# Kernel optimization log

Hardware: AMD Instinct MI355X
Metric: run time of the kernel (lower is better)

Reference implementation:

```python
import jax, jax.numpy as jnp
import numpy as np

B, S, H, D = 4, 2048, 16, 64
DM = H * D  # model dim 1024


def _rope_sincos(seq_len, d2):
    # sin/cos tables for the rotated sub-dimension d2 (= head_dim // 2)
    inv_freq = 1.0 / (10000.0 ** (jnp.arange(0, d2, 2, dtype=jnp.float32) / d2))
    ang = jnp.arange(seq_len, dtype=jnp.float32)[:, None] * inv_freq[None, :]  # (S, d2/2)
    emb = jnp.concatenate([ang, ang], axis=-1)  # (S, d2)
    return jnp.sin(emb), jnp.cos(emb)


def _apply_rope(x, sin, cos):
    # x: (B, S, H, D). Only the first half of head_dim is rotated (faithful to
    # apply_rotary_pos_emb: split -> rotate x1 -> concat with untouched x2).
    x1, x2 = jnp.split(x, 2, axis=-1)  # each (B, S, H, D//2)
    a, b = jnp.split(x1, 2, axis=-1)
    rot = jnp.concatenate([-b, a], axis=-1)  # rotate_half(x1)
    sin = sin[None, :, None, :]
    cos = cos[None, :, None, :]
    return jnp.concatenate([x1 * cos + rot * sin, x2], axis=-1)


def setup_inputs() -> dict:
    key = jax.random.key(0)
    k1, k2 = jax.random.split(key)
    x = jax.random.normal(k1, (B, S, DM), dtype=jnp.float32)
    w_qkv = jax.random.normal(k2, (DM, 3 * H * D), dtype=jnp.float32) / np.sqrt(DM).astype(np.float32)
    mask = jnp.tril(jnp.ones((1, 1, S, S), dtype=bool))  # causal
    return {"x": x, "w_qkv": w_qkv, "mask": mask}


def reference(x, w_qkv, mask):
    b, s, _ = x.shape
    qkv = x @ w_qkv  # (B, S, 3*H*D) fused QKV projection (no bias)
    q, k, v = jnp.split(qkv, 3, axis=-1)
    q = q.reshape(b, s, H, D)
    k = k.reshape(b, s, H, D)
    v = v.reshape(b, s, H, D)
    sin, cos = _rope_sincos(s, D // 2)
    q = _apply_rope(q, sin, cos)
    k = _apply_rope(k, sin, cos)
    # full (B, H, S, S) score matrix, scaled by sqrt(head_dim)
    attn = jnp.einsum('bqhd,bkhd->bhqk', q, k) / jnp.sqrt(jnp.float32(D))
    attn = jnp.where(mask, attn, -jnp.inf)
    attn = jax.nn.softmax(attn, axis=-1)
    out = jnp.einsum('bhqk,bkhd->bqhd', attn, v)
    return out.reshape(b, s, H * D)
```

## Files before the change

### kernel.cpp

```cpp
#include <hip/hip_runtime.h>
#include <hip/hip_bf16.h>

#define SEQ 2048
#define DM 1024
#define NOUT 3072

typedef __attribute__((ext_vector_type(8))) short bf16x8;
typedef __attribute__((ext_vector_type(4))) float f32x4;
typedef __attribute__((ext_vector_type(16))) float f32x16;
typedef __attribute__((ext_vector_type(4))) unsigned int u32x4;

__device__ inline unsigned short bfb(float f) {
    __hip_bfloat16 h = __float2bfloat16(f);
    return __builtin_bit_cast(unsigned short, h);
}

__device__ inline unsigned pk2(float lo, float hi) {
    return (unsigned)bfb(lo) | ((unsigned)bfb(hi) << 16);
}

__device__ inline void gload_lds16(const void* g, void* l) {
    __builtin_amdgcn_global_load_lds(
        (const __attribute__((address_space(1))) unsigned int*)g,
        (__attribute__((address_space(3))) unsigned int*)l, 16, 0, 0);
}

#define M3(a, b, c) fmaxf(fmaxf((a), (b)), (c))

__global__ __launch_bounds__(256) void prep_kernel(
    const float* __restrict__ x, __hip_bfloat16* __restrict__ xb,
    const float* __restrict__ w, __hip_bfloat16* __restrict__ wT,
    float* __restrict__ sintab, float* __restrict__ costab) {
    __shared__ float t[64][65];
    const int b = blockIdx.x, tid = threadIdx.x;
    if (b < 8192) {
        int i = b * 256 + tid;
        float4 v = ((const float4*)x)[i];
        ushort4 o;
        o.x = bfb(v.x); o.y = bfb(v.y); o.z = bfb(v.z); o.w = bfb(v.w);
        ((ushort4*)xb)[i] = o;
    } else if (b < 8960) {
        const int idx = b - 8192;
        const int k0 = (idx & 15) * 64;
        const int n0 = (idx >> 4) * 64;
        for (int i = tid; i < 4096; i += 256) {
            int r = i >> 6, c = i & 63;
            t[r][c] = w[(size_t)(k0 + r) * NOUT + n0 + c];
        }
        __syncthreads();
        for (int i = tid; i < 4096; i += 256) {
            int nl = i >> 6, kl = i & 63;
            wT[(size_t)(n0 + nl) * DM + k0 + kl] = __float2bfloat16(t[kl][nl]);
        }
    } else {
        int i = (b - 8960) * 256 + tid;
        int f = i & 15, s = i >> 4;
        float inv = powf(10000.0f, -(float)f * (1.0f / 16.0f));
        float ang = (float)s * inv;
        sintab[i] = sinf(ang);
        costab[i] = cosf(ang);
    }
}

#define BM 128
#define BN 128
#define BK 32

__global__ __launch_bounds__(256) void qkv_gemm_kernel(
    const __hip_bfloat16* __restrict__ xb, const __hip_bfloat16* __restrict__ wT,
    const float* __restrict__ costab, const float* __restrict__ sintab,
    __hip_bfloat16* __restrict__ Qg, __hip_bfloat16* __restrict__ Kg,
    __hip_bfloat16* __restrict__ Vt) {
    __shared__ __hip_bfloat16 As[BM * BK];
    __shared__ __hip_bfloat16 Bs[BN * BK];
    const int tid = threadIdx.x, lane = tid & 63, wid = tid >> 6;
    const int wm = wid >> 1, wn = wid & 1;
    const int m0 = blockIdx.x * BM, n0 = blockIdx.y * BN;
    const int g = lane >> 4;

    f32x4 acc[4][4] = {};

    for (int k0 = 0; k0 < DM; k0 += BK) {
        __syncthreads();
#pragma unroll
        for (int c2 = 0; c2 < 2; ++c2) {
            const int chunk = wid * 2 + c2;
            gload_lds16(xb + (size_t)(m0 + chunk * 16 + (lane >> 2)) * DM + k0 + (lane & 3) * 8,
                        &As[chunk * 512]);
            gload_lds16(wT + (size_t)(n0 + chunk * 16 + (lane >> 2)) * DM + k0 + (lane & 3) * 8,
                        &Bs[chunk * 512]);
        }
        __syncthreads();
        bf16x8 a[4], b[4];
#pragma unroll
        for (int mf = 0; mf < 4; ++mf)
            a[mf] = *(const bf16x8*)&As[(wm * 64 + mf * 16 + (lane & 15)) * BK + (g << 3)];
#pragma unroll
        for (int nf = 0; nf < 4; ++nf)
            b[nf] = *(const bf16x8*)&Bs[(wn * 64 + nf * 16 + (lane & 15)) * BK + (g << 3)];
#pragma unroll
        for (int mf = 0; mf < 4; ++mf)
#pragma unroll
            for (int nf = 0; nf < 4; ++nf)
                acc[mf][nf] = __builtin_amdgcn_mfma_f32_16x16x32_bf16(a[mf], b[nf], acc[mf][nf], 0, 0, 0);
    }

    const int colbase = n0 + wn * 64;
    const int part = colbase >> 10;
    const int h = (colbase & 1023) >> 6;
    const int d0 = lane & 15;
    const int rowg0 = m0 + wm * 64 + (g << 2);

    if (part == 2) {
#pragma unroll
        for (int mf = 0; mf < 4; ++mf) {
            const int rbase = rowg0 + mf * 16;
            const int b = rbase >> 11, s = rbase & 2047;
            const size_t vb = (size_t)(b * 16 + h) * 64 * SEQ;
#pragma unroll
            for (int nf = 0; nf < 4; ++nf) {
                const int d = nf * 16 + d0;
                ushort4 pk;
                pk.x = bfb(acc[mf][nf][0]);
                pk.y = bfb(acc[mf][nf][1]);
                pk.z = bfb(acc[mf][nf][2]);
                pk.w = bfb(acc[mf][nf][3]);
                *(ushort4*)((unsigned short*)Vt + vb + (size_t)d * SEQ + s) = pk;
            }
        }
    } else {
        __hip_bfloat16* __restrict__ dstT = part ? Kg : Qg;
        const float sc = part ? 1.0f : 0.125f * 1.44269504088896340736f;
#pragma unroll
        for (int mf = 0; mf < 4; ++mf) {
#pragma unroll
            for (int j = 0; j < 4; ++j) {
                const int mg = rowg0 + mf * 16 + j;
                const int b = mg >> 11, s = mg & 2047;
                const float cv = costab[s * 16 + d0];
                const float sv = sintab[s * 16 + d0];
                const float v0 = acc[mf][0][j], v1 = acc[mf][1][j];
                __hip_bfloat16* dst = dstT + ((size_t)(b * 16 + h) * SEQ + s) * 64;
                dst[d0]      = __float2bfloat16((v0 * cv - v1 * sv) * sc);
                dst[16 + d0] = __float2bfloat16((v1 * cv + v0 * sv) * sc);
                dst[32 + d0] = __float2bfloat16(acc[mf][2][j] * sc);
                dst[48 + d0] = __float2bfloat16(acc[mf][3][j] * sc);
            }
        }
    }
}

__global__ __launch_bounds__(512) void attn_fwd_kernel(
    const __hip_bfloat16* __restrict__ Qg, const __hip_bfloat16* __restrict__ Kg,
    const __hip_bfloat16* __restrict__ Vt, float* __restrict__ out) {
    __shared__ __align__(16) char smem[2][16384];
    const int tid = threadIdx.x, lane = tid & 63, wid = tid >> 6;
    const int qt = 7 - (blockIdx.x >> 6);
    const int bh = blockIdx.x & 63;
    const size_t base = (size_t)bh << 17;
    const int ql = lane & 31, hi = lane >> 5;
    const int qb = (qt << 8) + (wid << 5);
    const int qrow = qb + ql;
    const int nkt = 4 * qt + 4;
    const unsigned short* Kgu = (const unsigned short*)Kg + base;
    const unsigned short* Vtu = (const unsigned short*)Vt + base;
    const int b = bh >> 4, h = bh & 15;
    const int lo16 = lane << 4;

    bf16x8 qfrag[4];
    {
        const unsigned short* qp = (const unsigned short*)Qg + base + (size_t)qrow * 64 + hi * 8;
#pragma unroll
        for (int c = 0; c < 4; ++c) qfrag[c] = *(const bf16x8*)(qp + c * 16);
    }

    f32x16 accO[2] = {};
    float m = -INFINITY, l = 0.0f;

    const int ci0 = (wid & 3) * 2;
    const unsigned short* stsrc;
    int stdst;
    if (wid < 4) {
        stsrc = Kgu + (size_t)((ci0 >> 2) * 32 + ql) * 64 + (ci0 & 3) * 16 + hi * 8;
        stdst = ci0 * 1024;
    } else {
        stsrc = Vtu + (size_t)((ci0 >> 2) * 32 + ql) * SEQ + (ci0 & 3) * 16 + hi * 8;
        stdst = 8192 + ci0 * 1024;
    }

    {
#pragma unroll
        for (int c = 0; c < 2; ++c)
            gload_lds16(stsrc + c * 16, &smem[0][stdst + c * 1024]);
    }

    int cur = 0;
#pragma unroll 1
    for (int kt = 0; kt < nkt; ++kt) {
        const int k0 = kt << 6;
        if (kt + 1 < nkt) {
            const int kn = (kt + 1) << 6;
            const unsigned short* sn = (wid < 4) ? stsrc + (size_t)kn * 64 : stsrc + kn;
            char* nb = &smem[cur ^ 1][stdst];
#pragma unroll
            for (int c = 0; c < 2; ++c)
                gload_lds16(sn + c * 16, nb + c * 1024);
            asm volatile("s_waitcnt vmcnt(2)" ::: "memory");
        } else {
            asm volatile("s_waitcnt vmcnt(0)" ::: "memory");
        }
        __builtin_amdgcn_s_barrier();
        __builtin_amdgcn_sched_barrier(0);

        if (k0 <= qb + 31) {
            const char* Ks = smem[cur];
            const char* Vs = smem[cur] + 8192;

            f32x16 st[2] = {};
            __builtin_amdgcn_s_setprio(1);
#pragma unroll
            for (int c = 0; c < 4; ++c) {
                bf16x8 kf0 = *(const bf16x8*)(Ks + c * 1024 + lo16);
                bf16x8 kf1 = *(const bf16x8*)(Ks + 4096 + c * 1024 + lo16);
                st[0] = __builtin_amdgcn_mfma_f32_32x32x16_bf16(kf0, qfrag[c], st[0], 0, 0, 0);
                st[1] = __builtin_amdgcn_mfma_f32_32x32x16_bf16(kf1, qfrag[c], st[1], 0, 0, 0);
            }
            __builtin_amdgcn_s_setprio(0);

            if (k0 + 63 > qb) {
#pragma unroll
                for (int t = 0; t < 2; ++t)
#pragma unroll
                    for (int r = 0; r < 16; ++r) {
                        const int kg = k0 + 32 * t + (r & 3) + 8 * (r >> 2) + 4 * hi;
                        if (kg > qrow) st[t][r] = -INFINITY;
                    }
            }

            float x0 = M3(st[0][0], st[0][1], st[0][2]);
            float x1 = M3(st[0][3], st[0][4], st[0][5]);
            float x2 = M3(st[0][6], st[0][7], st[0][8]);
            float x3 = M3(st[0][9], st[0][10], st[0][11]);
            float x4 = M3(st[0][12], st[0][13], st[0][14]);
            float x5 = M3(st[0][15], st[1][0], st[1][1]);
            float x6 = M3(st[1][2], st[1][3], st[1][4]);
            float x7 = M3(st[1][5], st[1][6], st[1][7]);
            float x8 = M3(st[1][8], st[1][9], st[1][10]);
            float x9 = M3(st[1][11], st[1][12], st[1][13]);
            float xa = fmaxf(st[1][14], st[1][15]);
            float y0 = M3(x0, x1, x2), y1 = M3(x3, x4, x5);
            float y2 = M3(x6, x7, x8), y3 = M3(x9, xa, y0);
            float tm = M3(y1, y2, y3);
            tm = fmaxf(tm, __shfl_xor(tm, 32, 64));

            if (__any(tm > m + 8.0f)) {
                const float mn = fmaxf(m, tm);
                const float scl = __builtin_amdgcn_exp2f(m - mn);
                m = mn;
                l *= scl;
#pragma unroll
                for (int db = 0; db < 2; ++db)
#pragma unroll
                    for (int r = 0; r < 16; ++r) accO[db][r] *= scl;
            }

            float s0 = 0.0f, s1 = 0.0f, s2 = 0.0f, s3 = 0.0f;
#pragma unroll
            for (int r = 0; r < 16; r += 4) {
                float p00 = __builtin_amdgcn_exp2f(st[0][r + 0] - m);
                float p01 = __builtin_amdgcn_exp2f(st[0][r + 1] - m);
                float p02 = __builtin_amdgcn_exp2f(st[0][r + 2] - m);
                float p03 = __builtin_amdgcn_exp2f(st[0][r + 3] - m);
                float p10 = __builtin_amdgcn_exp2f(st[1][r + 0] - m);
                float p11 = __builtin_amdgcn_exp2f(st[1][r + 1] - m);
                float p12 = __builtin_amdgcn_exp2f(st[1][r + 2] - m);
                float p13 = __builtin_amdgcn_exp2f(st[1][r + 3] - m);
                st[0][r + 0] = p00; st[0][r + 1] = p01; st[0][r + 2] = p02; st[0][r + 3] = p03;
                st[1][r + 0] = p10; st[1][r + 1] = p11; st[1][r + 2] = p12; st[1][r + 3] = p13;
                s0 += p00 + p01; s1 += p02 + p03;
                s2 += p10 + p11; s3 += p12 + p13;
            }
            float ls = (s0 + s1) + (s2 + s3);
            ls += __shfl_xor(ls, 32, 64);
            l += ls;

            bf16x8 pfrag[4];
#pragma unroll
            for (int ks = 0; ks < 4; ++ks) {
                const int t = ks >> 1, rb = (ks & 1) * 8;
                unsigned a0 = pk2(st[t][rb + 0], st[t][rb + 1]);
                unsigned a1 = pk2(st[t][rb + 2], st[t][rb + 3]);
                unsigned b0 = pk2(st[t][rb + 4], st[t][rb + 5]);
                unsigned b1 = pk2(st[t][rb + 6], st[t][rb + 7]);
                asm("v_permlane32_swap_b32 %0, %1" : "+v"(a0), "+v"(b0));
                asm("v_permlane32_swap_b32 %0, %1" : "+v"(a1), "+v"(b1));
                u32x4 w;
                w[0] = a0;
                w[1] = a1;
                w[2] = b0;
                w[3] = b1;
                pfrag[ks] = __builtin_bit_cast(bf16x8, w);
            }

            __builtin_amdgcn_s_setprio(1);
#pragma unroll
            for (int ks = 0; ks < 4; ++ks) {
#pragma unroll
                for (int db = 0; db < 2; ++db) {
                    bf16x8 vf = *(const bf16x8*)(Vs + (db * 4 + ks) * 1024 + lo16);
                    accO[db] = __builtin_amdgcn_mfma_f32_32x32x16_bf16(vf, pfrag[ks], accO[db], 0, 0, 0);
                }
            }
            __builtin_amdgcn_s_setprio(0);
        }

        __builtin_amdgcn_sched_barrier(0);
        __builtin_amdgcn_s_barrier();
        cur ^= 1;
    }

    const float invl = 1.0f / l;
    float* orow = out + (size_t)(b * SEQ + qrow) * DM + h * 64;
#pragma unroll
    for (int db = 0; db < 2; ++db)
#pragma unroll
        for (int rg = 0; rg < 4; ++rg) {
            float4 v;
            v.x = accO[db][rg * 4 + 0] * invl;
            v.y = accO[db][rg * 4 + 1] * invl;
            v.z = accO[db][rg * 4 + 2] * invl;
            v.w = accO[db][rg * 4 + 3] * invl;
            *(float4*)(orow + db * 32 + rg * 8 + hi * 4) = v;
        }
}

extern "C" void kernel_launch(void* const* d_in, const int* in_sizes, int n_in,
                              void* d_out, int out_size, void* d_ws, size_t ws_size,
                              hipStream_t stream) {
    const float* x = (const float*)d_in[0];
    const float* w = (const float*)d_in[1];
    float* out = (float*)d_out;
    char* ws = (char*)d_ws;

    __hip_bfloat16* xb  = (__hip_bfloat16*)(ws + 0);
    __hip_bfloat16* wT  = (__hip_bfloat16*)(ws + 16777216);
    __hip_bfloat16* Qg  = (__hip_bfloat16*)(ws + 23068672);
    __hip_bfloat16* Kg  = (__hip_bfloat16*)(ws + 39845888);
    __hip_bfloat16* Vt  = (__hip_bfloat16*)(ws + 56623104);
    float* costab       = (float*)(ws + 73400320);
    float* sintab       = (float*)(ws + 73531392);

    prep_kernel<<<dim3(9088), dim3(256), 0, stream>>>(x, xb, w, wT, sintab, costab);
    qkv_gemm_kernel<<<dim3(64, 24), dim3(256), 0, stream>>>(xb, wT, costab, sintab, Qg, Kg, Vt);
    attn_fwd_kernel<<<dim3(512), dim3(512), 0, stream>>>(Qg, Kg, Vt, out);
}
```

Before: 141.6 us.

## Rewrite QKV GEMM as 256x256 double-buffered, swizzled, 8-wave pipelined kernel

Replaces the 128x128x32 single-buffered QKV projection GEMM with 256x256 tiles, BK=64, 8 waves and 128KB of dynamic LDS split into two buffers. Global-to-LDS loads for the next K step are issued in quarters between MFMA phases, with explicit vmcnt waits, barriers and raised priority around the MFMA blocks. An XOR swizzle is added to cut LDS bank conflicts. The aim is to hide load latency and increase data reuse per tile, at the cost of only 384 blocks (one per CU), which may leave CUs underused.

```diff
diff --git a/kernel.cpp b/kernel.cpp
--- a/kernel.cpp
+++ b/kernel.cpp
@@ -62,58 +62,151 @@
     }
 }
 
-#define BM 128
-#define BN 128
-#define BK 32
-
-__global__ __launch_bounds__(256) void qkv_gemm_kernel(
+#define QPERBUF 65536
+
+__global__ __launch_bounds__(512, 1) void qkv_gemm_kernel(
     const __hip_bfloat16* __restrict__ xb, const __hip_bfloat16* __restrict__ wT,
     const float* __restrict__ costab, const float* __restrict__ sintab,
     __hip_bfloat16* __restrict__ Qg, __hip_bfloat16* __restrict__ Kg,
     __hip_bfloat16* __restrict__ Vt) {
-    __shared__ __hip_bfloat16 As[BM * BK];
-    __shared__ __hip_bfloat16 Bs[BN * BK];
+    extern __shared__ __align__(16) char smc[];
     const int tid = threadIdx.x, lane = tid & 63, wid = tid >> 6;
-    const int wm = wid >> 1, wn = wid & 1;
-    const int m0 = blockIdx.x * BM, n0 = blockIdx.y * BN;
-    const int g = lane >> 4;
-
-    f32x4 acc[4][4] = {};
-
-    for (int k0 = 0; k0 < DM; k0 += BK) {
-        __syncthreads();
-#pragma unroll
-        for (int c2 = 0; c2 < 2; ++c2) {
-            const int chunk = wid * 2 + c2;
-            gload_lds16(xb + (size_t)(m0 + chunk * 16 + (lane >> 2)) * DM + k0 + (lane & 3) * 8,
-                        &As[chunk * 512]);
-            gload_lds16(wT + (size_t)(n0 + chunk * 16 + (lane >> 2)) * DM + k0 + (lane & 3) * 8,
-                        &Bs[chunk * 512]);
-        }
-        __syncthreads();
-        bf16x8 a[4], b[4];
-#pragma unroll
-        for (int mf = 0; mf < 4; ++mf)
-            a[mf] = *(const bf16x8*)&As[(wm * 64 + mf * 16 + (lane & 15)) * BK + (g << 3)];
-#pragma unroll
-        for (int nf = 0; nf < 4; ++nf)
-            b[nf] = *(const bf16x8*)&Bs[(wn * 64 + nf * 16 + (lane & 15)) * BK + (g << 3)];
-#pragma unroll
-        for (int mf = 0; mf < 4; ++mf)
-#pragma unroll
-            for (int nf = 0; nf < 4; ++nf)
-                acc[mf][nf] = __builtin_amdgcn_mfma_f32_16x16x32_bf16(a[mf], b[nf], acc[mf][nf], 0, 0, 0);
+    const int wm = wid >> 2, wn = wid & 3;
+    const int m0 = blockIdx.x * 256, n0 = blockIdx.y * 256;
+    const int l15 = lane & 15;
+
+    const int ak0 = (((lane >> 4) ^ (lane & 7)) << 4);
+    const int ak1 = (((4 + (lane >> 4)) ^ (lane & 7)) << 4);
+    const int Aoff = wm * 16384 + l15 * 128;
+    const int Boff = 32768 + (wn >> 1) * 16384 + (wn & 1) * 8192 + l15 * 128;
+
+    const int srow = lane >> 3;
+    const int skel = ((lane & 7) ^ srow) * 8;
+    const __hip_bfloat16* gA = xb + (size_t)(m0 + srow) * DM + skel;
+    const __hip_bfloat16* gB = wT + (size_t)(n0 + srow) * DM + skel;
+
+#define STAGE_A(h, l, kk, nb)                                                   \
+    gload_lds16(gA + (size_t)((h) * 128 + (l) * 64 + wid * 8) * DM + (kk),      \
+                smc + (nb) + (h) * 16384 + (l) * 8192 + wid * 1024)
+#define STAGE_B(h, l, kk, nb)                                                   \
+    gload_lds16(gB + (size_t)((h) * 128 + (l) * 64 + wid * 8) * DM + (kk),      \
+                smc + (nb) + 32768 + (h) * 16384 + (l) * 8192 + wid * 1024)
+
+    f32x4 acc[8][4] = {};
+    bf16x8 aR[4][2], bA[2][2], bB[2][2];
+
+    STAGE_A(0, 0, 0, 0); STAGE_A(0, 1, 0, 0);
+    STAGE_A(1, 0, 0, 0); STAGE_A(1, 1, 0, 0);
+    STAGE_B(0, 0, 0, 0); STAGE_B(0, 1, 0, 0);
+    STAGE_B(1, 0, 0, 0); STAGE_B(1, 1, 0, 0);
+
+#pragma unroll 1
+    for (int t = 0; t < 16; ++t) {
+        const int cb = (t & 1) * QPERBUF;
+        const int nb = cb ^ QPERBUF;
+        const int kk = (t + 1) * 64;
+        const char* Ab = smc + cb + Aoff;
+        const char* Bb = smc + cb + Boff;
+
+        if (t < 15) {
+            STAGE_A(0, 0, kk, nb); STAGE_A(0, 1, kk, nb);
+            asm volatile("s_waitcnt vmcnt(2)" ::: "memory");
+        } else {
+            asm volatile("s_waitcnt vmcnt(0)" ::: "memory");
+        }
+        __builtin_amdgcn_s_barrier();
+        __builtin_amdgcn_sched_barrier(0);
+#pragma unroll
+        for (int i = 0; i < 4; ++i) {
+            aR[i][0] = *(const bf16x8*)(Ab + i * 2048 + ak0);
+            aR[i][1] = *(const bf16x8*)(Ab + i * 2048 + ak1);
+        }
+#pragma unroll
+        for (int j = 0; j < 2; ++j) {
+            bA[j][0] = *(const bf16x8*)(Bb + j * 2048 + ak0);
+            bA[j][1] = *(const bf16x8*)(Bb + j * 2048 + ak1);
+        }
+        __builtin_amdgcn_s_setprio(1);
+#pragma unroll
+        for (int s = 0; s < 2; ++s)
+#pragma unroll
+            for (int i = 0; i < 4; ++i)
+#pragma unroll
+                for (int j = 0; j < 2; ++j)
+                    acc[i][j] = __builtin_amdgcn_mfma_f32_16x16x32_bf16(aR[i][s], bA[j][s], acc[i][j], 0, 0, 0);
+        __builtin_amdgcn_s_setprio(0);
+        __builtin_amdgcn_sched_barrier(0);
+        __builtin_amdgcn_s_barrier();
+        __builtin_amdgcn_sched_barrier(0);
+
+        if (t < 15) { STAGE_A(1, 0, kk, nb); STAGE_A(1, 1, kk, nb); }
+#pragma unroll
+        for (int j = 0; j < 2; ++j) {
+            bB[j][0] = *(const bf16x8*)(Bb + (2 + j) * 2048 + ak0);
+            bB[j][1] = *(const bf16x8*)(Bb + (2 + j) * 2048 + ak1);
+        }
+        __builtin_amdgcn_s_setprio(1);
+#pragma unroll
+        for (int s = 0; s < 2; ++s)
+#pragma unroll
+            for (int i = 0; i < 4; ++i)
+#pragma unroll
+                for (int j = 0; j < 2; ++j)
+                    acc[i][2 + j] = __builtin_amdgcn_mfma_f32_16x16x32_bf16(aR[i][s], bB[j][s], acc[i][2 + j], 0, 0, 0);
+        __builtin_amdgcn_s_setprio(0);
+        __builtin_amdgcn_sched_barrier(0);
+        __builtin_amdgcn_s_barrier();
+        __builtin_amdgcn_sched_barrier(0);
+
+        if (t < 15) { STAGE_B(0, 0, kk, nb); STAGE_B(0, 1, kk, nb); }
+#pragma unroll
+        for (int i = 0; i < 4; ++i) {
+            aR[i][0] = *(const bf16x8*)(Ab + (4 + i) * 2048 + ak0);
+            aR[i][1] = *(const bf16x8*)(Ab + (4 + i) * 2048 + ak1);
+        }
+#pragma unroll
+        for (int j = 0; j < 2; ++j) {
+            bA[j][0] = *(const bf16x8*)(Bb + j * 2048 + ak0);
+            bA[j][1] = *(const bf16x8*)(Bb + j * 2048 + ak1);
+        }
+        __builtin_amdgcn_s_setprio(1);
+#pragma unroll
+        for (int s = 0; s < 2; ++s)
+#pragma unroll
+            for (int i = 0; i < 4; ++i)
+#pragma unroll
+                for (int j = 0; j < 2; ++j)
+                    acc[4 + i][j] = __builtin_amdgcn_mfma_f32_16x16x32_bf16(aR[i][s], bA[j][s], acc[4 + i][j], 0, 0, 0);
+        __builtin_amdgcn_s_setprio(0);
+        __builtin_amdgcn_sched_barrier(0);
+        __builtin_amdgcn_s_barrier();
+        __builtin_amdgcn_sched_barrier(0);
+
+        if (t < 15) { STAGE_B(1, 0, kk, nb); STAGE_B(1, 1, kk, nb); }
+        __builtin_amdgcn_s_setprio(1);
+#pragma unroll
+        for (int s = 0; s < 2; ++s)
+#pragma unroll
+            for (int i = 0; i < 4; ++i)
+#pragma unroll
+                for (int j = 0; j < 2; ++j)
+                    acc[4 + i][2 + j] = __builtin_amdgcn_mfma_f32_16x16x32_bf16(aR[i][s], bB[j][s], acc[4 + i][2 + j], 0, 0, 0);
+        __builtin_amdgcn_s_setprio(0);
+        __builtin_amdgcn_sched_barrier(0);
+        __builtin_amdgcn_s_barrier();
+        __builtin_amdgcn_sched_barrier(0);
     }
 
     const int colbase = n0 + wn * 64;
     const int part = colbase >> 10;
     const int h = (colbase & 1023) >> 6;
     const int d0 = lane & 15;
-    const int rowg0 = m0 + wm * 64 + (g << 2);
+    const int g = lane >> 4;
+    const int rowg0 = m0 + wm * 128 + (g << 2);
 
     if (part == 2) {
 #pragma unroll
-        for (int mf = 0; mf < 4; ++mf) {
+        for (int mf = 0; mf < 8; ++mf) {
             const int rbase = rowg0 + mf * 16;
             const int b = rbase >> 11, s = rbase & 2047;
             const size_t vb = (size_t)(b * 16 + h) * 64 * SEQ;
@@ -132,7 +225,7 @@
         __hip_bfloat16* __restrict__ dstT = part ? Kg : Qg;
         const float sc = part ? 1.0f : 0.125f * 1.44269504088896340736f;
 #pragma unroll
-        for (int mf = 0; mf < 4; ++mf) {
+        for (int mf = 0; mf < 8; ++mf) {
 #pragma unroll
             for (int j = 0; j < 4; ++j) {
                 const int mg = rowg0 + mf * 16 + j;
@@ -350,7 +443,14 @@
     float* costab       = (float*)(ws + 73400320);
     float* sintab       = (float*)(ws + 73531392);
 
+    static bool qkv_attr_set = false;
+    if (!qkv_attr_set) {
+        hipFuncSetAttribute((const void*)qkv_gemm_kernel,
+                            hipFuncAttributeMaxDynamicSharedMemorySize, 131072);
+        qkv_attr_set = true;
+    }
+
     prep_kernel<<<dim3(9088), dim3(256), 0, stream>>>(x, xb, w, wT, sintab, costab);
-    qkv_gemm_kernel<<<dim3(64, 24), dim3(256), 0, stream>>>(xb, wT, costab, sintab, Qg, Kg, Vt);
+    qkv_gemm_kernel<<<dim3(32, 12), dim3(512), 131072, stream>>>(xb, wT, costab, sintab, Qg, Kg, Vt);
     attn_fwd_kernel<<<dim3(512), dim3(512), 0, stream>>>(Qg, Kg, Vt, out);
 }
```

Result: slower. 146.0 us (+3.1%).
